# Performance work log

Hardware: AMD Instinct MI355X
Metric: run time of the kernel (lower is better)

Reference implementation:

```python
import jax, jax.numpy as jnp
import numpy as np

N_NODES = 65536
N_EDGES = 1048576
F_IN = 128
HEADS = 4
HID = 64
N_GRAPHS = 1024
NODES_PER_GRAPH = N_NODES // N_GRAPHS
EPS = 1e-5
NEG_SLOPE = 0.2


def setup_inputs() -> dict:
    key = jax.random.key(0)
    ks = jax.random.split(key, 8)
    x = jax.random.normal(ks[0], (N_NODES, F_IN), dtype=jnp.float32)
    edge_index = jax.random.randint(ks[1], (2, N_EDGES), 0, N_NODES, dtype=jnp.int64)
    batch = (jnp.arange(N_NODES, dtype=jnp.int64) // NODES_PER_GRAPH)
    s = 1.0 / np.sqrt(F_IN)
    w_l = jax.random.normal(ks[2], (HEADS * HID, F_IN), dtype=jnp.float32) * s
    w_r = jax.random.normal(ks[3], (HEADS * HID, F_IN), dtype=jnp.float32) * s
    att = jax.random.normal(ks[4], (HEADS, HID), dtype=jnp.float32) * (1.0 / np.sqrt(HID))
    return {
        "x": x,
        "edge_index": edge_index,
        "batch": batch,
        "num_graphs": N_GRAPHS,
        "bn_gamma": jnp.ones((F_IN,), jnp.float32),
        "bn_beta": jnp.zeros((F_IN,), jnp.float32),
        "w_l": w_l,
        "b_l": jnp.zeros((HEADS * HID,), jnp.float32),
        "w_r": w_r,
        "b_r": jnp.zeros((HEADS * HID,), jnp.float32),
        "att": att,
        "bias": jnp.zeros((HID,), jnp.float32),
    }


def reference(x, edge_index, batch, num_graphs, bn_gamma, bn_beta,
              w_l, b_l, w_r, b_r, att, bias):
    N = x.shape[0]
    H, C = att.shape
    # BatchNorm1d (training-mode: batch stats, biased variance)
    mean = jnp.mean(x, axis=0)
    var = jnp.var(x, axis=0)
    xn = (x - mean) * jax.lax.rsqrt(var + EPS) * bn_gamma + bn_beta
    # GATv2Conv: separate src/dst linear transforms
    xs = (xn @ w_l.T + b_l).reshape(N, H, C)
    xd = (xn @ w_r.T + b_r).reshape(N, H, C)
    # add self-loops (PyG default)
    loop = jnp.arange(N, dtype=edge_index.dtype)
    src = jnp.concatenate([edge_index[0], loop])
    dst = jnp.concatenate([edge_index[1], loop])
    # per-edge messages and GATv2 attention logits
    msg = xs[src]                               # [E, H, C]
    e = jax.nn.leaky_relu(msg + xd[dst], NEG_SLOPE)
    logits = jnp.einsum('ehc,hc->eh', e, att)    # [E, H]
    # segment-wise (per-destination) softmax
    m = jax.ops.segment_max(logits, dst, num_segments=N)
    p = jnp.exp(logits - m[dst])
    s = jax.ops.segment_sum(p, dst, num_segments=N)
    alpha = p / s[dst]                           # [E, H]
    # scatter-aggregate weighted messages
    out = jax.ops.segment_sum(alpha[:, :, None] * msg, dst, num_segments=N)  # [N,H,C]
    out = out.mean(axis=1) + bias                # concat=False -> mean over heads
    out = jax.nn.elu(out)
    return out.reshape(num_graphs, -1, C)
```

## Files before the change

### kernel.cpp

```cpp
#include <hip/hip_runtime.h>
#include <hip/hip_bf16.h>

#define N_NODES 65536
#define N_EDGES 1048576
#define F_IN    128
#define HEADS   4
#define HID     64
#define NHID    256
#define NBUCK   1024
#define BCAP    2048

typedef float fx4 __attribute__((ext_vector_type(4)));
typedef short bf16x8 __attribute__((ext_vector_type(8)));
typedef float f32x4 __attribute__((ext_vector_type(4)));
typedef float f32x2 __attribute__((ext_vector_type(2)));

typedef __attribute__((address_space(1))) const unsigned as1_cuint;
typedef __attribute__((address_space(3))) unsigned as3_uint;

__device__ inline unsigned short f2bf(float f) {
    unsigned u = __float_as_uint(f);
    u += 0x7fff + ((u >> 16) & 1);
    return (unsigned short)(u >> 16);
}
__device__ inline float bf2f(unsigned short h) {
    return __uint_as_float((unsigned)h << 16);
}
__device__ inline float bflo(unsigned w) { return __uint_as_float(w << 16); }
__device__ inline float bfhi(unsigned w) { return __uint_as_float(w & 0xffff0000u); }

template <int CTRL>
__device__ inline float dpp_add(float x) {
    int y = __builtin_amdgcn_update_dpp(0, __float_as_int(x), CTRL, 0xf, 0xf, true);
    return x + __int_as_float(y);
}

__global__ __launch_bounds__(256) void k_bn_stats(const float* __restrict__ x,
                                                  float* __restrict__ sums,
                                                  unsigned short* __restrict__ xhi) {
    const int t = threadIdx.x;
    const int lane = t & 63;
    const int w = t >> 6;
    const int wid = blockIdx.x * 4 + w;
    float s0 = 0.f, s1 = 0.f, q0 = 0.f, q1 = 0.f;
    for (int i = 0; i < 64; ++i) {
        int r = wid + i * 1024;
        float2 v = *(const float2*)(x + (size_t)r * F_IN + lane * 2);
        s0 += v.x; q0 += v.x * v.x;
        s1 += v.y; q1 += v.y * v.y;
        unsigned short h0 = f2bf(v.x), h1 = f2bf(v.y);
        int slot = (lane >> 2) ^ (r & 7);
        int idx = r * 64 + slot * 4 + (lane & 3);
        ((unsigned*)xhi)[idx] = (unsigned)h0 | ((unsigned)h1 << 16);
    }
    __shared__ float sh[4][128];
    sh[w][lane * 2] = s0; sh[w][lane * 2 + 1] = s1;
    __syncthreads();
    if (t < 128) atomicAdd(&sums[t], sh[0][t] + sh[1][t] + sh[2][t] + sh[3][t]);
    __syncthreads();
    sh[w][lane * 2] = q0; sh[w][lane * 2 + 1] = q1;
    __syncthreads();
    if (t < 128) atomicAdd(&sums[128 + t], sh[0][t] + sh[1][t] + sh[2][t] + sh[3][t]);
}

__global__ void k_bn_finalize(const float* __restrict__ sums,
                              const float* __restrict__ gamma,
                              const float* __restrict__ beta,
                              const float* __restrict__ att,
                              float* __restrict__ scale,
                              float* __restrict__ shift,
                              float* __restrict__ att_l2e) {
    int t = threadIdx.x;
    float mean = sums[t] * (1.0f / N_NODES);
    float var  = sums[128 + t] * (1.0f / N_NODES) - mean * mean;
    float sc = gamma[t] * rsqrtf(var + 1e-5f);
    scale[t] = sc;
    shift[t] = beta[t] - mean * sc;
    att_l2e[t]       = att[t]       * 1.44269504088896f;
    att_l2e[t + 128] = att[t + 128] * 1.44269504088896f;
}

__global__ __launch_bounds__(256) void k_prep_w(const float* __restrict__ w_l,
                                                const float* __restrict__ b_l,
                                                const float* __restrict__ w_r,
                                                const float* __restrict__ b_r,
                                                const float* __restrict__ scale,
                                                const float* __restrict__ shift,
                                                unsigned short* __restrict__ Whi,
                                                unsigned short* __restrict__ Wlo,
                                                float* __restrict__ bp) {
    const int t = threadIdx.x;
    const int lane = t & 63;
    const int o = blockIdx.x * 4 + (t >> 6);
    const float* wrow = (o < NHID) ? (w_l + (size_t)o * F_IN)
                                   : (w_r + (size_t)(o - NHID) * F_IN);
    float bo = (o < NHID) ? b_l[o] : b_r[o - NHID];
    float2 wv = *(const float2*)(wrow + lane * 2);
    float w0 = wv.x * scale[lane * 2], w1 = wv.y * scale[lane * 2 + 1];
    unsigned short h0 = f2bf(w0), h1 = f2bf(w1);
    unsigned short l0 = f2bf(w0 - bf2f(h0)), l1 = f2bf(w1 - bf2f(h1));
    int slot = (lane >> 2) ^ (o & 7);
    int idx = o * 64 + slot * 4 + (lane & 3);
    ((unsigned*)Whi)[idx] = (unsigned)h0 | ((unsigned)h1 << 16);
    ((unsigned*)Wlo)[idx] = (unsigned)l0 | ((unsigned)l1 << 16);
    float part = shift[lane * 2] * wv.x + shift[lane * 2 + 1] * wv.y;
    #pragma unroll
    for (int m = 1; m < 64; m <<= 1) part += __shfl_xor(part, m, 64);
    if (lane == 0) bp[o] = bo + part;
}

__global__ __launch_bounds__(512) void k_gemm_mfma(const unsigned short* __restrict__ xhi,
                                                   const unsigned short* __restrict__ Whi,
                                                   const unsigned short* __restrict__ Wlo,
                                                   const float* __restrict__ bp,
                                                   unsigned short* __restrict__ xs_bf,
                                                   unsigned short* __restrict__ xd_bf) {
    __shared__ __align__(16) char lds[98304];
    const int t = threadIdx.x;
    const int bid = blockIdx.x;
    const int mb = (bid & 7) * 64 + ((bid >> 3) >> 2);
    const int nb = (bid >> 3) & 3;
    const int m0 = mb * 128, n0 = nb * 128;
    {
        const unsigned* srcs[3] = {
            (const unsigned*)(xhi + (size_t)m0 * 128),
            (const unsigned*)(Whi + (size_t)n0 * 128),
            (const unsigned*)(Wlo + (size_t)n0 * 128)};
        #pragma unroll
        for (int c = 0; c < 3; ++c) {
            #pragma unroll
            for (int q = 0; q < 4; ++q) {
                int i = (q * 512 + t) * 4;
                __builtin_amdgcn_global_load_lds(
                    (as1_cuint*)(srcs[c] + i),
                    (as3_uint*)(lds + c * 32768 + i * 4),
                    16, 0, 0);
            }
        }
    }
    __syncthreads();
    const int wvi = t >> 6, lane = t & 63;
    const int wm = wvi >> 2, wn = wvi & 3;
    const int lg = lane >> 4, lr = lane & 15;
    f32x4 acc[4][2] = {};
    #pragma unroll
    for (int ks = 0; ks < 4; ++ks) {
        bf16x8 ah[4], bh[2], bl[2];
        #pragma unroll
        for (int mi = 0; mi < 4; ++mi) {
            int r = wm * 64 + mi * 16 + lr;
            int off = r * 256 + ((((ks << 2) + lg) ^ (r & 7)) << 4);
            ah[mi] = *(const bf16x8*)(lds + off);
        }
        #pragma unroll
        for (int nj = 0; nj < 2; ++nj) {
            int r = wn * 32 + nj * 16 + lr;
            int off = r * 256 + ((((ks << 2) + lg) ^ (r & 7)) << 4);
            bh[nj] = *(const bf16x8*)(lds + 32768 + off);
            bl[nj] = *(const bf16x8*)(lds + 65536 + off);
        }
        #pragma unroll
        for (int mi = 0; mi < 4; ++mi)
            #pragma unroll
            for (int nj = 0; nj < 2; ++nj) {
                acc[mi][nj] = __builtin_amdgcn_mfma_f32_16x16x32_bf16(ah[mi], bh[nj], acc[mi][nj], 0, 0, 0);
                acc[mi][nj] = __builtin_amdgcn_mfma_f32_16x16x32_bf16(ah[mi], bl[nj], acc[mi][nj], 0, 0, 0);
            }
    }
    unsigned short* outp = (n0 < NHID) ? xs_bf : xd_bf;
    const int ncol0 = n0 & 255;
    #pragma unroll
    for (int nj = 0; nj < 2; ++nj) {
        int nc = wn * 32 + nj * 16 + lr;
        float bcol = bp[n0 + nc];
        #pragma unroll
        for (int mi = 0; mi < 4; ++mi) {
            #pragma unroll
            for (int r = 0; r < 4; ++r) {
                int m = m0 + wm * 64 + mi * 16 + lg * 4 + r;
                outp[(size_t)m * NHID + ncol0 + nc] = f2bf(acc[mi][nj][r] + bcol);
            }
        }
    }
}

__global__ __launch_bounds__(256) void k_coarse(const int* __restrict__ ei,
                                                int* __restrict__ ccnt,
                                                unsigned* __restrict__ cbuf) {
    __shared__ int cnt[NBUCK];
    __shared__ int base[NBUCK];
    const int t = threadIdx.x;
    for (int i = t; i < NBUCK; i += 256) cnt[i] = 0;
    __syncthreads();
    const int e0 = blockIdx.x * 4096;
    int myrank[16];
    #pragma unroll
    for (int k = 0; k < 16; ++k) {
        int d = ei[N_EDGES + e0 + k * 256 + t];
        myrank[k] = atomicAdd(&cnt[d >> 6], 1);
    }
    __syncthreads();
    for (int i = t; i < NBUCK; i += 256)
        base[i] = (i << 11) + atomicAdd(&ccnt[i], cnt[i]);
    __syncthreads();
    #pragma unroll
    for (int k = 0; k < 16; ++k) {
        int e = e0 + k * 256 + t;
        int s = ei[e];
        int d = ei[N_EDGES + e];
        unsigned pos = (unsigned)(base[d >> 6] + myrank[k]);
        if ((pos >> 11) == (unsigned)(d >> 6))
            cbuf[pos] = (unsigned)s | ((unsigned)(d & 63) << 16);
    }
}

__global__ __launch_bounds__(256) void k_fineA(const unsigned* __restrict__ cbuf,
                                               const int* __restrict__ ccnt,
                                               int* __restrict__ counts) {
    __shared__ int nc[64];
    const int t = threadIdx.x;
    const int b = blockIdx.x;
    if (t < 64) nc[t] = 0;
    __syncthreads();
    const int cnt = min(ccnt[b], BCAP);
    const unsigned* p = cbuf + (size_t)b * BCAP;
    for (int e = t; e < cnt; e += 256)
        atomicAdd(&nc[(p[e] >> 16) & 63], 1);
    __syncthreads();
    if (t < 64) counts[b * 64 + t] = nc[t];
}

__global__ __launch_bounds__(256) void k_scan1(const int* __restrict__ counts,
                                               int* __restrict__ row_start,
                                               int* __restrict__ blocksums) {
    __shared__ int sh[256];
    int t = threadIdx.x;
    int i = blockIdx.x * 256 + t;
    int v = counts[i];
    sh[t] = v;
    __syncthreads();
    for (int off = 1; off < 256; off <<= 1) {
        int add = (t >= off) ? sh[t - off] : 0;
        __syncthreads();
        sh[t] += add;
        __syncthreads();
    }
    row_start[i] = sh[t] - v;
    if (t == 255) blocksums[blockIdx.x] = sh[255];
}

__global__ void k_scan2(int* __restrict__ blocksums) {
    __shared__ int sh[256];
    int t = threadIdx.x;
    int v = blocksums[t];
    sh[t] = v;
    __syncthreads();
    for (int off = 1; off < 256; off <<= 1) {
        int add = (t >= off) ? sh[t - off] : 0;
        __syncthreads();
        sh[t] += add;
        __syncthreads();
    }
    blocksums[t] = sh[t] - v;
}

__global__ __launch_bounds__(256) void k_scan3(int* __restrict__ row_start,
                                               const int* __restrict__ blocksums) {
    int i = blockIdx.x * 256 + threadIdx.x;
    row_start[i] += blocksums[blockIdx.x];
}

__global__ __launch_bounds__(256) void k_fineB(const unsigned* __restrict__ cbuf,
                                               const int* __restrict__ ccnt,
                                               const int* __restrict__ row_start,
                                               int* __restrict__ csr) {
    __shared__ int rs[64];
    __shared__ int cur[64];
    const int t = threadIdx.x;
    const int b = blockIdx.x;
    if (t < 64) { rs[t] = row_start[b * 64 + t]; cur[t] = 0; }
    __syncthreads();
    const int cnt = min(ccnt[b], BCAP);
    const unsigned* p = cbuf + (size_t)b * BCAP;
    for (int e = t; e < cnt; e += 256) {
        unsigned w2 = p[e];
        int d = (w2 >> 16) & 63;
        int r = atomicAdd(&cur[d], 1);
        csr[rs[d] + r] = (int)(w2 & 0xffffu);
    }
}

__global__ __launch_bounds__(256) void k_aggregate(const unsigned short* __restrict__ xs_bf,
                                                   const unsigned short* __restrict__ xd_bf,
                                                   const int* __restrict__ row_start,
                                                   const int* __restrict__ counts,
                                                   const int* __restrict__ csr,
                                                   const float* __restrict__ att_l2e,
                                                   const float* __restrict__ bias,
                                                   float* __restrict__ out) {
    const int t = threadIdx.x;
    const int lane = t & 63;
    const int node  = __builtin_amdgcn_readfirstlane(blockIdx.x * 4 + (t >> 6));
    const int start = __builtin_amdgcn_readfirstlane(row_start[node]);
    const int deg   = __builtin_amdgcn_readfirstlane(counts[node]);
    const int total = deg + 1;

    f32x2 att01, att23, xd01, xd23;
    {
        float4 a = *(const float4*)(att_l2e + lane * 4);
        att01.x = 0.6f * a.x; att01.y = 0.6f * a.y;
        att23.x = 0.6f * a.z; att23.y = 0.6f * a.w;
        uint2 xw = *(const uint2*)(xd_bf + (size_t)node * NHID + lane * 4);
        xd01.x = bflo(xw.x); xd01.y = bfhi(xw.x);
        xd23.x = bflo(xw.y); xd23.y = bfhi(xw.y);
    }

    const char* xsb = (const char*)xs_bf;
    const unsigned voff = (unsigned)lane * 8;
    float ssumA = 0.f, ssumB = 0.f;
    f32x2 accA01 = {0.f, 0.f}, accA23 = {0.f, 0.f};
    f32x2 accB01 = {0.f, 0.f}, accB23 = {0.f, 0.f};

#define LDX(S) (*(const uint2*)(xsb + (((size_t)(unsigned)(S)) << 9) + voff))
#define LOGIT(U, DD) {                                                         \
        f32x2 c01, c23;                                                        \
        c01.x = bflo((U).x); c01.y = bfhi((U).x);                              \
        c23.x = bflo((U).y); c23.y = bfhi((U).y);                              \
        f32x2 sv01 = c01 + xd01, sv23 = c23 + xd23;                            \
        f32x2 dA2 = att01 * c01 + att23 * c23;                                 \
        f32x2 a01v, a23v;                                                      \
        a01v.x = fabsf(sv01.x); a01v.y = fabsf(sv01.y);                        \
        a23v.x = fabsf(sv23.x); a23v.y = fabsf(sv23.y);                        \
        f32x2 dB2 = att01 * a01v + att23 * a23v;                               \
        DD = fmaf(0.66666667f, dB2.x + dB2.y, dA2.x + dA2.y);                  \
        DD = dpp_add<0xB1>(DD);                                                \
        DD = dpp_add<0x4E>(DD);                                                \
        DD = dpp_add<0x141>(DD);                                               \
        DD = dpp_add<0x140>(DD); }
#define ACCUM(U, P, SS, A01, A23) {                                            \
        f32x2 c01, c23;                                                        \
        c01.x = bflo((U).x); c01.y = bfhi((U).x);                              \
        c23.x = bflo((U).y); c23.y = bfhi((U).y);                              \
        SS += P;                                                               \
        f32x2 p2 = {P, P};                                                     \
        A01 += p2 * c01; A23 += p2 * c23; }
#define PROC_NC(U, SS, A01, A23) {                                             \
        float d_;                                                              \
        LOGIT(U, d_)                                                           \
        float p_ = __builtin_amdgcn_exp2f(d_);                                 \
        ACCUM(U, p_, SS, A01, A23) }
#define PROC_C(U, KOFF, SS, A01, A23) {                                        \
        float d_;                                                              \
        LOGIT(U, d_)                                                           \
        if (j + (KOFF) >= cnt) d_ = -1e30f;                                    \
        float p_ = __builtin_amdgcn_exp2f(d_);                                 \
        ACCUM(U, p_, SS, A01, A23) }

    for (int base = 0; base < total; base += 64) {
        const int cnt = __builtin_amdgcn_readfirstlane(min(64, total - base));
        int item = base + lane;
        int idx = node;
        if ((unsigned)(item - 1) < (unsigned)deg)
            idx = csr[start + item - 1];
        uint2 c0 = LDX(__builtin_amdgcn_readlane(idx, 0));
        uint2 c1 = LDX(__builtin_amdgcn_readlane(idx, 1));
        uint2 c2 = LDX(__builtin_amdgcn_readlane(idx, 2));
        uint2 c3 = LDX(__builtin_amdgcn_readlane(idx, 3));
        int j = 0;
        for (; j + 4 <= cnt; j += 4) {
            uint2 u0 = c0, u1 = c1, u2 = c2, u3 = c3;
            if (j + 4 < cnt) {
                c0 = LDX(__builtin_amdgcn_readlane(idx, j + 4));
                c1 = LDX(__builtin_amdgcn_readlane(idx, j + 5));
                c2 = LDX(__builtin_amdgcn_readlane(idx, j + 6));
                c3 = LDX(__builtin_amdgcn_readlane(idx, j + 7));
            }
            PROC_NC(u0, ssumA, accA01, accA23)
            PROC_NC(u1, ssumB, accB01, accB23)
            PROC_NC(u2, ssumA, accA01, accA23)
            PROC_NC(u3, ssumB, accB01, accB23)
        }
        if (j < cnt) {
            uint2 u0 = c0, u1 = c1, u2 = c2, u3 = c3;
            PROC_C(u0, 0, ssumA, accA01, accA23)
            PROC_C(u1, 1, ssumB, accB01, accB23)
            PROC_C(u2, 2, ssumA, accA01, accA23)
            PROC_C(u3, 3, ssumB, accB01, accB23)
        }
    }
#undef PROC_C
#undef PROC_NC
#undef ACCUM
#undef LOGIT
#undef LDX

    float ssum = ssumA + ssumB;
    f32x2 acc01 = accA01 + accB01;
    f32x2 acc23 = accA23 + accB23;

    float inv = __builtin_amdgcn_rcpf(ssum);
    float r0 = acc01.x * inv, r1 = acc01.y * inv;
    float r2 = acc23.x * inv, r3 = acc23.y * inv;
    r0 += __shfl_xor(r0, 16, 64); r0 += __shfl_xor(r0, 32, 64);
    r1 += __shfl_xor(r1, 16, 64); r1 += __shfl_xor(r1, 32, 64);
    r2 += __shfl_xor(r2, 16, 64); r2 += __shfl_xor(r2, 32, 64);
    r3 += __shfl_xor(r3, 16, 64); r3 += __shfl_xor(r3, 32, 64);
    if (lane < 16) {
        float4 b4 = *(const float4*)(bias + lane * 4);
        float o0 = r0 * 0.25f + b4.x;
        float o1 = r1 * 0.25f + b4.y;
        float o2 = r2 * 0.25f + b4.z;
        float o3 = r3 * 0.25f + b4.w;
        o0 = (o0 > 0.f) ? o0 : __builtin_amdgcn_exp2f(o0 * 1.44269504f) - 1.0f;
        o1 = (o1 > 0.f) ? o1 : __builtin_amdgcn_exp2f(o1 * 1.44269504f) - 1.0f;
        o2 = (o2 > 0.f) ? o2 : __builtin_amdgcn_exp2f(o2 * 1.44269504f) - 1.0f;
        o3 = (o3 > 0.f) ? o3 : __builtin_amdgcn_exp2f(o3 * 1.44269504f) - 1.0f;
        float4 o = {o0, o1, o2, o3};
        *(float4*)(out + (size_t)node * HID + lane * 4) = o;
    }
}

extern "C" void kernel_launch(void* const* d_in, const int* in_sizes, int n_in,
                              void* d_out, int out_size, void* d_ws, size_t ws_size,
                              hipStream_t stream) {
    const float* x     = (const float*)d_in[0];
    const int*   ei    = (const int*)d_in[1];
    const float* gamma = (const float*)d_in[4];
    const float* beta  = (const float*)d_in[5];
    const float* w_l   = (const float*)d_in[6];
    const float* b_l   = (const float*)d_in[7];
    const float* w_r   = (const float*)d_in[8];
    const float* b_r   = (const float*)d_in[9];
    const float* att   = (const float*)d_in[10];
    const float* bias  = (const float*)d_in[11];
    float* out = (float*)d_out;

    char* ws = (char*)d_ws;
    unsigned short* xs_bf = (unsigned short*)ws;
    unsigned short* xd_bf = xs_bf + (size_t)N_NODES * NHID;
    unsigned short* xhi   = xd_bf + (size_t)N_NODES * NHID;
    unsigned short* Whi   = xhi + (size_t)N_NODES * F_IN;
    unsigned short* Wlo   = Whi + 512 * F_IN;
    float* bp      = (float*)(Wlo + 512 * F_IN);
    float* scale   = bp + 512;
    float* shift   = scale + 128;
    float* att_l2e = shift + 128;
    float* sums    = att_l2e + 256;
    int* counts    = (int*)(sums + 256);
    int* ccnt      = counts + N_NODES;
    int* row_start = ccnt + NBUCK;
    int* blocksums = row_start + N_NODES;
    int* csr       = blocksums + 256;
    unsigned* cbuf = (unsigned*)(csr + N_EDGES);

    (void)hipMemsetAsync(sums, 0, (256 + N_NODES + NBUCK) * sizeof(float), stream);

    k_bn_stats<<<256, 256, 0, stream>>>(x, sums, xhi);
    k_bn_finalize<<<1, 128, 0, stream>>>(sums, gamma, beta, att, scale, shift, att_l2e);
    k_prep_w<<<128, 256, 0, stream>>>(w_l, b_l, w_r, b_r, scale, shift, Whi, Wlo, bp);
    k_gemm_mfma<<<2048, 512, 0, stream>>>(xhi, Whi, Wlo, bp, xs_bf, xd_bf);

    k_coarse<<<N_EDGES / 4096, 256, 0, stream>>>(ei, ccnt, cbuf);
    k_fineA<<<NBUCK, 256, 0, stream>>>(cbuf, ccnt, counts);
    k_scan1<<<256, 256, 0, stream>>>(counts, row_start, blocksums);
    k_scan2<<<1, 256, 0, stream>>>(blocksums);
    k_scan3<<<256, 256, 0, stream>>>(row_start, blocksums);
    k_fineB<<<NBUCK, 256, 0, stream>>>(cbuf, ccnt, row_start, csr);

    k_aggregate<<<N_NODES / 4, 256, 0, stream>>>(xs_bf, xd_bf, row_start, counts, csr,
                                                 att_l2e, bias, out);
}
```

Before: 175.7 us.

## Fuse CSR build into bucket scan plus single fine pass; stage GEMM stores via LDS

Replaces the five CSR-construction kernels (fineA, three-level scan, fineB) with one bucket-level scan and one fused fine kernel. The fused kernel computes per-node counts and ranks in registers, scans row starts within the block with wave shuffles, and scatters into the CSR in a single read of the bucket buffer. The GEMM epilogue now stages bf16 outputs in LDS and writes 16-byte coalesced rows instead of scattered 2-byte stores. The aggregation macros are merged without changing behavior, and the memset shrinks because counts no longer need zeroing. Together this cuts launch count, cbuf rereads, and uncoalesced global writes, at the cost of an extra LDS round trip and two barriers in the GEMM.

```diff
diff --git a/kernel.cpp b/kernel.cpp
--- a/kernel.cpp
+++ b/kernel.cpp
@@ -167,20 +167,36 @@
                 acc[mi][nj] = __builtin_amdgcn_mfma_f32_16x16x32_bf16(ah[mi], bl[nj], acc[mi][nj], 0, 0, 0);
             }
     }
-    unsigned short* outp = (n0 < NHID) ? xs_bf : xd_bf;
-    const int ncol0 = n0 & 255;
+    __syncthreads();
+    unsigned short* cs = (unsigned short*)lds;
     #pragma unroll
     for (int nj = 0; nj < 2; ++nj) {
         int nc = wn * 32 + nj * 16 + lr;
         float bcol = bp[n0 + nc];
         #pragma unroll
         for (int mi = 0; mi < 4; ++mi) {
+            int row = wm * 64 + mi * 16 + lg * 4;
             #pragma unroll
-            for (int r = 0; r < 4; ++r) {
-                int m = m0 + wm * 64 + mi * 16 + lg * 4 + r;
-                outp[(size_t)m * NHID + ncol0 + nc] = f2bf(acc[mi][nj][r] + bcol);
-            }
-        }
+            for (int r = 0; r < 4; ++r)
+                cs[(row + r) * 132 + nc] = f2bf(acc[mi][nj][r] + bcol);
+        }
+    }
+    __syncthreads();
+    {
+        unsigned short* outp = (n0 < NHID) ? xs_bf : xd_bf;
+        const int ncol0 = n0 & 255;
+        int row = t >> 2;
+        int cseg = (t & 3) * 32;
+        const unsigned short* src = cs + row * 132 + cseg;
+        unsigned short* dst = outp + (size_t)(m0 + row) * NHID + ncol0 + cseg;
+        uint4 v0 = *(const uint4*)(src);
+        uint4 v1 = *(const uint4*)(src + 8);
+        uint4 v2 = *(const uint4*)(src + 16);
+        uint4 v3 = *(const uint4*)(src + 24);
+        *(uint4*)(dst)      = v0;
+        *(uint4*)(dst + 8)  = v1;
+        *(uint4*)(dst + 16) = v2;
+        *(uint4*)(dst + 24) = v3;
     }
 }
 
@@ -214,30 +230,13 @@
     }
 }
 
-__global__ __launch_bounds__(256) void k_fineA(const unsigned* __restrict__ cbuf,
-                                               const int* __restrict__ ccnt,
-                                               int* __restrict__ counts) {
-    __shared__ int nc[64];
-    const int t = threadIdx.x;
-    const int b = blockIdx.x;
-    if (t < 64) nc[t] = 0;
-    __syncthreads();
-    const int cnt = min(ccnt[b], BCAP);
-    const unsigned* p = cbuf + (size_t)b * BCAP;
-    for (int e = t; e < cnt; e += 256)
-        atomicAdd(&nc[(p[e] >> 16) & 63], 1);
-    __syncthreads();
-    if (t < 64) counts[b * 64 + t] = nc[t];
-}
-
-__global__ __launch_bounds__(256) void k_scan1(const int* __restrict__ counts,
-                                               int* __restrict__ row_start,
-                                               int* __restrict__ blocksums) {
+__global__ __launch_bounds__(256) void k_scanb(const int* __restrict__ ccnt,
+                                               int* __restrict__ cbase) {
     __shared__ int sh[256];
     int t = threadIdx.x;
-    int i = blockIdx.x * 256 + t;
-    int v = counts[i];
-    sh[t] = v;
+    int4 v = *(const int4*)(ccnt + t * 4);
+    int s = v.x + v.y + v.z + v.w;
+    sh[t] = s;
     __syncthreads();
     for (int off = 1; off < 256; off <<= 1) {
         int add = (t >= off) ? sh[t - off] : 0;
@@ -245,48 +244,59 @@
         sh[t] += add;
         __syncthreads();
     }
-    row_start[i] = sh[t] - v;
-    if (t == 255) blocksums[blockIdx.x] = sh[255];
-}
-
-__global__ void k_scan2(int* __restrict__ blocksums) {
-    __shared__ int sh[256];
-    int t = threadIdx.x;
-    int v = blocksums[t];
-    sh[t] = v;
-    __syncthreads();
-    for (int off = 1; off < 256; off <<= 1) {
-        int add = (t >= off) ? sh[t - off] : 0;
-        __syncthreads();
-        sh[t] += add;
-        __syncthreads();
-    }
-    blocksums[t] = sh[t] - v;
-}
-
-__global__ __launch_bounds__(256) void k_scan3(int* __restrict__ row_start,
-                                               const int* __restrict__ blocksums) {
-    int i = blockIdx.x * 256 + threadIdx.x;
-    row_start[i] += blocksums[blockIdx.x];
-}
-
-__global__ __launch_bounds__(256) void k_fineB(const unsigned* __restrict__ cbuf,
-                                               const int* __restrict__ ccnt,
-                                               const int* __restrict__ row_start,
-                                               int* __restrict__ csr) {
-    __shared__ int rs[64];
-    __shared__ int cur[64];
+    int e = sh[t] - s;
+    cbase[t * 4 + 0] = e; e += v.x;
+    cbase[t * 4 + 1] = e; e += v.y;
+    cbase[t * 4 + 2] = e; e += v.z;
+    cbase[t * 4 + 3] = e;
+}
+
+__global__ __launch_bounds__(256) void k_fine(const unsigned* __restrict__ cbuf,
+                                              const int* __restrict__ ccnt,
+                                              const int* __restrict__ cbase,
+                                              int* __restrict__ counts,
+                                              int* __restrict__ row_start,
+                                              int* __restrict__ csr) {
+    __shared__ int nc[64];
+    __shared__ int rowst[64];
     const int t = threadIdx.x;
     const int b = blockIdx.x;
-    if (t < 64) { rs[t] = row_start[b * 64 + t]; cur[t] = 0; }
+    if (t < 64) nc[t] = 0;
     __syncthreads();
     const int cnt = min(ccnt[b], BCAP);
     const unsigned* p = cbuf + (size_t)b * BCAP;
-    for (int e = t; e < cnt; e += 256) {
-        unsigned w2 = p[e];
-        int d = (w2 >> 16) & 63;
-        int r = atomicAdd(&cur[d], 1);
-        csr[rs[d] + r] = (int)(w2 & 0xffffu);
+    unsigned w2[8];
+    int rank[8];
+    #pragma unroll
+    for (int k = 0; k < 8; ++k) {
+        int e = t + k * 256;
+        if (e < cnt) {
+            w2[k] = p[e];
+            rank[k] = atomicAdd(&nc[(w2[k] >> 16) & 63], 1);
+        }
+    }
+    __syncthreads();
+    if (t < 64) {
+        int v = nc[t];
+        counts[b * 64 + t] = v;
+        int inc = v;
+        #pragma unroll
+        for (int off = 1; off < 64; off <<= 1) {
+            int n = __shfl_up(inc, off, 64);
+            if (t >= off) inc += n;
+        }
+        int rs = cbase[b] + inc - v;
+        row_start[b * 64 + t] = rs;
+        rowst[t] = rs;
+    }
+    __syncthreads();
+    #pragma unroll
+    for (int k = 0; k < 8; ++k) {
+        int e = t + k * 256;
+        if (e < cnt) {
+            int d = (w2[k] >> 16) & 63;
+            csr[rowst[d] + rank[k]] = (int)(w2[k] & 0xffffu);
+        }
     }
 }
 
@@ -322,7 +332,7 @@
     f32x2 accB01 = {0.f, 0.f}, accB23 = {0.f, 0.f};
 
 #define LDX(S) (*(const uint2*)(xsb + (((size_t)(unsigned)(S)) << 9) + voff))
-#define LOGIT(U, DD) {                                                         \
+#define PROC(U, GUARD, KOFF, SS, A01, A23) {                                   \
         f32x2 c01, c23;                                                        \
         c01.x = bflo((U).x); c01.y = bfhi((U).x);                              \
         c23.x = bflo((U).y); c23.y = bfhi((U).y);                              \
@@ -332,29 +342,16 @@
         a01v.x = fabsf(sv01.x); a01v.y = fabsf(sv01.y);                        \
         a23v.x = fabsf(sv23.x); a23v.y = fabsf(sv23.y);                        \
         f32x2 dB2 = att01 * a01v + att23 * a23v;                               \
-        DD = fmaf(0.66666667f, dB2.x + dB2.y, dA2.x + dA2.y);                  \
-        DD = dpp_add<0xB1>(DD);                                                \
-        DD = dpp_add<0x4E>(DD);                                                \
-        DD = dpp_add<0x141>(DD);                                               \
-        DD = dpp_add<0x140>(DD); }
-#define ACCUM(U, P, SS, A01, A23) {                                            \
-        f32x2 c01, c23;                                                        \
-        c01.x = bflo((U).x); c01.y = bfhi((U).x);                              \
-        c23.x = bflo((U).y); c23.y = bfhi((U).y);                              \
-        SS += P;                                                               \
-        f32x2 p2 = {P, P};                                                     \
+        float d_ = fmaf(0.66666667f, dB2.x + dB2.y, dA2.x + dA2.y);            \
+        d_ = dpp_add<0xB1>(d_);                                                \
+        d_ = dpp_add<0x4E>(d_);                                                \
+        d_ = dpp_add<0x141>(d_);                                               \
+        d_ = dpp_add<0x140>(d_);                         \
+        if (GUARD && j + (KOFF) >= cnt) d_ = -1e30f;                           \
+        float p_ = __builtin_amdgcn_exp2f(d_);                                 \
+        SS += p_;                                                              \
+        f32x2 p2 = {p_, p_};                                                   \
         A01 += p2 * c01; A23 += p2 * c23; }
-#define PROC_NC(U, SS, A01, A23) {                                             \
-        float d_;                                                              \
-        LOGIT(U, d_)                                                           \
-        float p_ = __builtin_amdgcn_exp2f(d_);                                 \
-        ACCUM(U, p_, SS, A01, A23) }
-#define PROC_C(U, KOFF, SS, A01, A23) {                                        \
-        float d_;                                                              \
-        LOGIT(U, d_)                                                           \
-        if (j + (KOFF) >= cnt) d_ = -1e30f;                                    \
-        float p_ = __builtin_amdgcn_exp2f(d_);                                 \
-        ACCUM(U, p_, SS, A01, A23) }
 
     for (int base = 0; base < total; base += 64) {
         const int cnt = __builtin_amdgcn_readfirstlane(min(64, total - base));
@@ -375,23 +372,20 @@
                 c2 = LDX(__builtin_amdgcn_readlane(idx, j + 6));
                 c3 = LDX(__builtin_amdgcn_readlane(idx, j + 7));
             }
-            PROC_NC(u0, ssumA, accA01, accA23)
-            PROC_NC(u1, ssumB, accB01, accB23)
-            PROC_NC(u2, ssumA, accA01, accA23)
-            PROC_NC(u3, ssumB, accB01, accB23)
+            PROC(u0, false, 0, ssumA, accA01, accA23)
+            PROC(u1, false, 1, ssumB, accB01, accB23)
+            PROC(u2, false, 2, ssumA, accA01, accA23)
+            PROC(u3, false, 3, ssumB, accB01, accB23)
         }
         if (j < cnt) {
             uint2 u0 = c0, u1 = c1, u2 = c2, u3 = c3;
-            PROC_C(u0, 0, ssumA, accA01, accA23)
-            PROC_C(u1, 1, ssumB, accB01, accB23)
-            PROC_C(u2, 2, ssumA, accA01, accA23)
-            PROC_C(u3, 3, ssumB, accB01, accB23)
-        }
-    }
-#undef PROC_C
-#undef PROC_NC
-#undef ACCUM
-#undef LOGIT
+            PROC(u0, true, 0, ssumA, accA01, accA23)
+            PROC(u1, true, 1, ssumB, accB01, accB23)
+            PROC(u2, true, 2, ssumA, accA01, accA23)
+            PROC(u3, true, 3, ssumB, accB01, accB23)
+        }
+    }
+#undef PROC
 #undef LDX
 
     float ssum = ssumA + ssumB;
@@ -446,14 +440,14 @@
     float* shift   = scale + 128;
     float* att_l2e = shift + 128;
     float* sums    = att_l2e + 256;
-    int* counts    = (int*)(sums + 256);
-    int* ccnt      = counts + N_NODES;
-    int* row_start = ccnt + NBUCK;
-    int* blocksums = row_start + N_NODES;
-    int* csr       = blocksums + 256;
+    int* ccnt      = (int*)(sums + 256);
+    int* cbase     = ccnt + NBUCK;
+    int* counts    = cbase + NBUCK;
+    int* row_start = counts + N_NODES;
+    int* csr       = row_start + N_NODES;
     unsigned* cbuf = (unsigned*)(csr + N_EDGES);
 
-    (void)hipMemsetAsync(sums, 0, (256 + N_NODES + NBUCK) * sizeof(float), stream);
+    (void)hipMemsetAsync(sums, 0, (256 + NBUCK) * sizeof(float), stream);
 
     k_bn_stats<<<256, 256, 0, stream>>>(x, sums, xhi);
     k_bn_finalize<<<1, 128, 0, stream>>>(sums, gamma, beta, att, scale, shift, att_l2e);
@@ -461,11 +455,8 @@
     k_gemm_mfma<<<2048, 512, 0, stream>>>(xhi, Whi, Wlo, bp, xs_bf, xd_bf);
 
     k_coarse<<<N_EDGES / 4096, 256, 0, stream>>>(ei, ccnt, cbuf);
-    k_fineA<<<NBUCK, 256, 0, stream>>>(cbuf, ccnt, counts);
-    k_scan1<<<256, 256, 0, stream>>>(counts, row_start, blocksums);
-    k_scan2<<<1, 256, 0, stream>>>(blocksums);
-    k_scan3<<<256, 256, 0, stream>>>(row_start, blocksums);
-    k_fineB<<<NBUCK, 256, 0, stream>>>(cbuf, ccnt, row_start, csr);
+    k_scanb<<<1, 256, 0, stream>>>(ccnt, cbase);
+    k_fine<<<NBUCK, 256, 0, stream>>>(cbuf, ccnt, cbase, counts, row_start, csr);
 
     k_aggregate<<<N_NODES / 4, 256, 0, stream>>>(xs_bf, xd_bf, row_start, counts, csr,
                                                  att_l2e, bias, out);
```

After: 185.0 us. 5.3% more time.
